# Optimization experiments

Hardware: AMD Instinct MI355X
Metric: run time of the kernel (lower is better)

The kernel has to match this reference:

```python
import jax, jax.numpy as jnp
import numpy as np

B, N, C = 32, 64, 128   # events, particles/event, channels (hidden==hidden2==out)
NUM_MAPS = 15           # bell_number(2+2)
E = B * N * N
LN_EPS = 1e-5


def setup_inputs() -> dict:
    key = jax.random.key(0)
    ks = jax.random.split(key, 8)
    x = jax.random.normal(ks[0], (E, C), jnp.float32)
    # complete graph with self-loops per event, nodes of event b are b*N..b*N+N-1
    node = np.arange(B * N, dtype=np.int32).reshape(B, N)
    src = np.repeat(node, N, axis=1).reshape(-1)            # i index per edge
    dst = np.tile(node, (1, N)).reshape(-1)                 # j index per edge
    edge_index = jnp.asarray(np.stack([src, dst]), jnp.int32)
    batch = jnp.asarray(np.repeat(np.arange(B, dtype=np.int32), N))
    # params: Linear(C->C), LayerNorm(C), factorized aggregator coeffs
    W_in = jax.random.normal(ks[1], (C, C), jnp.float32) / np.sqrt(C)
    b_in = jnp.zeros((C,), jnp.float32)
    ln_g = jnp.ones((C,), jnp.float32)
    ln_b = jnp.zeros((C,), jnp.float32)
    s0 = np.sqrt(3.0 / NUM_MAPS)
    s1 = np.sqrt(3.0 / C)
    c00 = jax.random.uniform(ks[2], (C, NUM_MAPS), jnp.float32, -s0, s0)
    c01 = jax.random.uniform(ks[3], (C, NUM_MAPS), jnp.float32, -s0, s0)
    c10 = jax.random.uniform(ks[4], (C, C), jnp.float32, -s1, s1)
    c11 = jax.random.uniform(ks[5], (C, C), jnp.float32, -s1, s1)
    return {"x": x, "edge_index": edge_index, "batch": batch,
            "W_in": W_in, "b_in": b_in, "ln_g": ln_g, "ln_b": ln_b,
            "c00": c00, "c01": c01, "c10": c10, "c11": c11}


def reference(x, edge_index, batch, W_in, b_in, ln_g, ln_b, c00, c01, c10, c11):
    # mlp: Linear -> GELU -> LayerNorm (this order, per ModuleList)
    h = x @ W_in.T + b_in
    h = jax.nn.gelu(h, approximate=False)
    mu = h.mean(-1, keepdims=True)
    var = ((h - mu) ** 2).mean(-1, keepdims=True)
    h = (h - mu) / jnp.sqrt(var + LN_EPS) * ln_g + ln_b

    # aggregate_2to2 with reduce='mean': 15 Eq(2->2) permutation-equivariant maps.
    # edge_index/batch describe complete graphs of N nodes per event -> dense view.
    t = h.reshape(B, N, N, C)                 # t[b,i,j,c]
    row = t.mean(axis=2)                      # [B,N,C] mean_j t[b,i,j]
    col = t.mean(axis=1)                      # [B,N,C] mean_i t[b,i,j]
    idx = jnp.arange(N)
    diag = t[:, idx, idx]                     # [B,N,C]
    trace = diag.mean(axis=1)                 # [B,C]
    tot = t.mean(axis=(1, 2))                 # [B,C]
    eye = jnp.eye(N, dtype=t.dtype)[None, :, :, None]

    # factorized coeffs [C_in?, C_out?, 15]; with C_in==C_out the flatten/linear in
    # the torch code makes the FIRST axis the output channel: out = sum map_m @ coeffs[:,:,m].T
    coeffs = c00[:, None, :] * c10[:, :, None] + c01[None, :, :] * c11[:, :, None]

    def proj(a, m):  # a[..., c] -> [..., o] with W[o, c] = coeffs[o, c, m]
        return jnp.einsum('...c,oc->...o', a, coeffs[:, :, m])

    out = proj(t, 0) + proj(t.swapaxes(1, 2), 1)
    out = out + proj(diag, 2)[:, :, None, :] + proj(diag, 3)[:, None, :, :]
    out = out + proj(row, 4)[:, :, None, :] + proj(row, 5)[:, None, :, :]
    out = out + proj(col, 6)[:, :, None, :] + proj(col, 7)[:, None, :, :]
    out = out + proj(trace, 8)[:, None, None, :] + proj(tot, 9)[:, None, None, :]
    out = out + eye * (proj(diag, 10)[:, :, None, :]
                       + proj(row, 11)[:, :, None, :]
                       + proj(col, 12)[:, :, None, :])
    out = out + eye * (proj(trace, 13)[:, None, None, :]
                       + proj(tot, 14)[:, None, None, :])

    return jax.nn.gelu(out.reshape(E, C), approximate=False)
```

## Files before the change

kernel.cpp:

```cpp
#include <hip/hip_runtime.h>
#include <hip/hip_bf16.h>


#define B_ 32
#define N_ 64
#define C_ 128
#define E_ (B_ * N_ * N_)
#define LN_EPS 1e-5f

typedef unsigned int u32;
typedef unsigned short u16;
typedef short bf16x8 __attribute__((ext_vector_type(8)));
typedef float f32x16 __attribute__((ext_vector_type(16)));

union FragU { uint4 u; bf16x8 v; };

__device__ inline float bf_u16(u16 u) { return __uint_as_float(((u32)u) << 16); }
__device__ inline u32 pack_bf2(float a, float b) {
    __hip_bfloat16 ha = __float2bfloat16(a), hb = __float2bfloat16(b);
    u16 ra = *reinterpret_cast<u16*>(&ha), rb = *reinterpret_cast<u16*>(&hb);
    return (u32)ra | ((u32)rb << 16);
}
__device__ inline u16 pack_bf1(float a) {
    __hip_bfloat16 ha = __float2bfloat16(a);
    return *reinterpret_cast<u16*>(&ha);
}
__device__ inline float b2f(__hip_bfloat16 v) { return __bfloat162float(v); }
__device__ inline float geluf(float v) {
    float v3 = v * v * v;
    float z = 0.7978845608f * fmaf(0.044715f, v3, v);
    float az = fabsf(z);
    float e = __expf(2.0f * az);
    float th = 1.0f - 2.0f / (e + 1.0f);
    th = copysignf(th, z);
    return 0.5f * v * (1.0f + th);
}
__device__ inline float ld1(const void* p, int i, int isbf) {
    if (isbf) return b2f(((const __hip_bfloat16*)p)[i]);
    return ((const float*)p)[i];
}
__device__ inline int bf_flag(const void* gp) {
    return (((const u32*)gp)[0] == 0x3F803F80u) ? 1 : 0;
}

#define O_T      ((size_t)0)
#define O_ROW    ((size_t)33554432)
#define O_DIAG   ((size_t)35651584)
#define O_CT     ((size_t)36732928)
#define O_WF     ((size_t)37715968)
#define O_CF     ((size_t)37748736)
#define O_U      ((size_t)37912576)
#define O_V      ((size_t)38961152)
#define O_DGN    ((size_t)40026112)
#define O_TT     ((size_t)41091328)

__global__ void pack_all(const void* __restrict__ W,
                         const void* __restrict__ c00, const void* __restrict__ c01,
                         const void* __restrict__ c10, const void* __restrict__ c11,
                         const void* __restrict__ gp,
                         uint4* __restrict__ WF, uint4* __restrict__ CF,
                         float* __restrict__ cT) {
    int isbf = bf_flag(gp);
    if (blockIdx.x < 24) {
        int idx = blockIdx.x * 256 + threadIdx.x;
        if (idx < 2048) {
            int l = idx & 63, s = (idx >> 6) & 7, ot = idx >> 9;
            int n = ot * 32 + (l & 31), k0 = s * 16 + (l >> 5) * 8;
            float v[8];
#pragma unroll
            for (int j = 0; j < 8; ++j) v[j] = ld1(W, n * 128 + k0 + j, isbf);
            uint4 o;
            o.x = pack_bf2(v[0], v[1]); o.y = pack_bf2(v[2], v[3]);
            o.z = pack_bf2(v[4], v[5]); o.w = pack_bf2(v[6], v[7]);
            WF[(s * 4 + ot) * 64 + l] = o;
        } else {
            int id2 = idx - 2048;
            int mat = id2 >> 11, r = id2 & 2047;
            int l = r & 63, s = (r >> 6) & 7, ot = r >> 9;
            int n = ot * 32 + (l & 31), k0 = s * 16 + (l >> 5) * 8;
            float v[8];
#pragma unroll
            for (int j = 0; j < 8; ++j) {
                int k = k0 + j;
                v[j] = ld1(c00, n * 15 + mat, isbf) * ld1(c10, n * 128 + k, isbf) +
                       ld1(c01, k * 15 + mat, isbf) * ld1(c11, n * 128 + k, isbf);
            }
            uint4 o;
            o.x = pack_bf2(v[0], v[1]); o.y = pack_bf2(v[2], v[3]);
            o.z = pack_bf2(v[4], v[5]); o.w = pack_bf2(v[6], v[7]);
            CF[mat * 2048 + (s * 4 + ot) * 64 + l] = o;
        }
    } else {
        int idx2 = (blockIdx.x - 24) * 256 + threadIdx.x;
        int m = idx2 >> 14, rem = idx2 & 16383;
        int c = rem >> 7, o = rem & 127;
        float val = ld1(c00, o * 15 + m, isbf) * ld1(c10, o * 128 + c, isbf) +
                    ld1(c01, c * 15 + m, isbf) * ld1(c11, o * 128 + c, isbf);
        cT[(m * 128 + c) * 128 + o] = val;
    }
}

__global__ void __launch_bounds__(256) gemm_ln_mfma(const void* __restrict__ x,
                                                    const uint4* __restrict__ WF,
                                                    const void* __restrict__ bp, const void* __restrict__ gp,
                                                    const void* __restrict__ lbp,
                                                    u16* __restrict__ t, u16* __restrict__ tT,
                                                    float* __restrict__ row_sum, float* __restrict__ diag) {
    __shared__ __align__(16) u16 tls[128 * 128];
    __shared__ float rsbuf[4][128];
    uint4* wfl = (uint4*)tls;
    int w = threadIdx.x >> 6, l = threadIdx.x & 63;
    int m = l & 31, hh = l >> 5;
    int isbf = bf_flag(gp);
    int e0 = blockIdx.x * 128;
    int arow = e0 + w * 32 + m;

#pragma unroll
    for (int k = 0; k < 8; ++k) {
        int idx = k * 256 + threadIdx.x;
        wfl[idx] = WF[idx];
    }

    FragU af[8];
    if (isbf) {
#pragma unroll
        for (int s = 0; s < 8; ++s)
            af[s].u = *(const uint4*)((const u16*)x + arow * 128 + s * 16 + hh * 8);
    } else {
        const float* xf = (const float*)x;
#pragma unroll
        for (int s = 0; s < 8; ++s) {
            int k0 = s * 16 + hh * 8;
            float4 f0 = *(const float4*)(xf + arow * 128 + k0);
            float4 f1 = *(const float4*)(xf + arow * 128 + k0 + 4);
            af[s].u.x = pack_bf2(f0.x, f0.y); af[s].u.y = pack_bf2(f0.z, f0.w);
            af[s].u.z = pack_bf2(f1.x, f1.y); af[s].u.w = pack_bf2(f1.z, f1.w);
        }
    }
    __syncthreads();

    f32x16 acc[4];
#pragma unroll
    for (int ot = 0; ot < 4; ++ot)
#pragma unroll
        for (int r = 0; r < 16; ++r) acc[ot][r] = 0.f;

#pragma unroll
    for (int s = 0; s < 8; ++s) {
#pragma unroll
        for (int ot = 0; ot < 4; ++ot) {
            FragU bf;
            bf.u = wfl[(s * 4 + ot) * 64 + l];
            acc[ot] = __builtin_amdgcn_mfma_f32_32x32x16_bf16(af[s].v, bf.v, acc[ot], 0, 0, 0);
        }
    }

    float bias[4], gsc[4], bof[4];
#pragma unroll
    for (int ot = 0; ot < 4; ++ot) {
        int o = ot * 32 + m;
        bias[ot] = ld1(bp, o, isbf);
        gsc[ot] = ld1(gp, o, isbf);
        bof[ot] = ld1(lbp, o, isbf);
    }
#pragma unroll
    for (int ot = 0; ot < 4; ++ot)
#pragma unroll
        for (int r = 0; r < 16; ++r) acc[ot][r] = geluf(acc[ot][r] + bias[ot]);

    __syncthreads();

    float rsum[4] = {0.f, 0.f, 0.f, 0.f};
#pragma unroll
    for (int r = 0; r < 16; ++r) {
        float s = acc[0][r] + acc[1][r] + acc[2][r] + acc[3][r];
        float s2 = acc[0][r] * acc[0][r] + acc[1][r] * acc[1][r] +
                   acc[2][r] * acc[2][r] + acc[3][r] * acc[3][r];
#pragma unroll
        for (int off = 1; off < 32; off <<= 1) {
            s += __shfl_xor(s, off);
            s2 += __shfl_xor(s2, off);
        }
        float mean = s * (1.0f / 128.0f);
        float var = s2 * (1.0f / 128.0f) - mean * mean;
        float rstd = rsqrtf(var + LN_EPS);
        int row = (r & 3) + 8 * (r >> 2) + 4 * hh;
#pragma unroll
        for (int ot = 0; ot < 4; ++ot) {
            int o = ot * 32 + m;
            float y = (acc[ot][r] - mean) * rstd * gsc[ot] + bof[ot];
            rsum[ot] += y;
            tls[(w * 32 + row) * 128 + o] = pack_bf1(y);
        }
    }
#pragma unroll
    for (int ot = 0; ot < 4; ++ot) {
        rsum[ot] += __shfl_xor(rsum[ot], 32);
        rsbuf[w][ot * 32 + m] = rsum[ot];
    }
    __syncthreads();

    int b = e0 >> 12, i0 = (e0 >> 6) & 63;
    {
        int p = threadIdx.x >> 7, c = threadIdx.x & 127;
        int ni = b * 64 + i0 + p;
        row_sum[ni * 128 + c] = rsbuf[2 * p][c] + rsbuf[2 * p + 1][c];
        diag[ni * 128 + c] = bf_u16(tls[(p * 64 + i0 + p) * 128 + c]);
    }
#pragma unroll
    for (int q = 0; q < 8; ++q) {
        int chunk = q * 256 + threadIdx.x;
        int row = chunk >> 4, c16 = chunk & 15;
        uint4 v = *(const uint4*)&tls[row * 128 + c16 * 8];
        *(uint4*)&t[(e0 + row) * 128 + c16 * 8] = v;
        int p = row >> 6, j = row & 63;
        int g = (b << 12) + (j << 6) + (i0 + p);
        *(uint4*)&tT[g * 128 + c16 * 8] = v;
    }
}

__global__ void __launch_bounds__(512) uvall_kernel(const u16* __restrict__ tT,
                                                    const float* __restrict__ row_sum,
                                                    const float* __restrict__ diag,
                                                    const float* __restrict__ cT,
                                                    float* __restrict__ U, float* __restrict__ V,
                                                    float* __restrict__ DgN) {
    __shared__ float dg[4][128], rm[4][128], cm[4][128];
    __shared__ float trs[128], tts[128];
    __shared__ float pU[4][4][128], pV[4][4][128], pD[4][4][128];
    __shared__ float paw[4][128], pad_[4][128];
    int b = blockIdx.x >> 4, n0 = (blockIdx.x & 15) * 4;
    int tid = threadIdx.x;
    int o = tid & 127, cq = tid >> 7;

    {
        int g = (b * 64 + n0 + cq) * 128 + o;
        dg[cq][o] = diag[g];
        rm[cq][o] = row_sum[g] * (1.0f / 64.0f);
    }
    float cs[4];
#pragma unroll
    for (int nn = 0; nn < 4; ++nn) {
        int base = ((b << 12) + ((n0 + nn) << 6) + cq * 16) * 128 + o;
        float s = 0.f;
#pragma unroll
        for (int i = 0; i < 16; ++i) s += bf_u16(tT[base + i * 128]);
        cs[nn] = s;
    }
    float tr = 0.f, tt = 0.f;
#pragma unroll
    for (int n = 0; n < 16; ++n) {
        int g = (b * 64 + cq * 16 + n) * 128 + o;
        tr += diag[g];
        tt += row_sum[g];
    }
#pragma unroll
    for (int nn = 0; nn < 4; ++nn) pU[cq][nn][o] = cs[nn];
    paw[cq][o] = tr;
    pad_[cq][o] = tt;
    __syncthreads();
    cm[cq][o] = (pU[0][cq][o] + pU[1][cq][o] + pU[2][cq][o] + pU[3][cq][o]) * (1.0f / 64.0f);
    if (cq == 0) trs[o] = (paw[0][o] + paw[1][o] + paw[2][o] + paw[3][o]) * (1.0f / 64.0f);
    if (cq == 1) tts[o] = (pad_[0][o] + pad_[1][o] + pad_[2][o] + pad_[3][o]) * (1.0f / 4096.0f);
    __syncthreads();

    float aU[4] = {0}, aV[4] = {0}, aD[4] = {0}, aw = 0.f, ad = 0.f;
    int c0 = cq * 32;
    for (int cc = 0; cc < 32; ++cc) {
        int c = c0 + cc;
        float c2 = cT[(2 * 128 + c) * 128 + o], c4 = cT[(4 * 128 + c) * 128 + o], c6 = cT[(6 * 128 + c) * 128 + o];
        float c3 = cT[(3 * 128 + c) * 128 + o], c5 = cT[(5 * 128 + c) * 128 + o], c7 = cT[(7 * 128 + c) * 128 + o];
        float cA = cT[(10 * 128 + c) * 128 + o], cB = cT[(11 * 128 + c) * 128 + o], cC = cT[(12 * 128 + c) * 128 + o];
        float c8 = cT[(8 * 128 + c) * 128 + o], c9 = cT[(9 * 128 + c) * 128 + o];
        float cD = cT[(13 * 128 + c) * 128 + o], cE = cT[(14 * 128 + c) * 128 + o];
        float trv = trs[c], ttv = tts[c];
        aw += c8 * trv + c9 * ttv;
        ad += cD * trv + cE * ttv;
#pragma unroll
        for (int nn = 0; nn < 4; ++nn) {
            float d = dg[nn][c], r = rm[nn][c], cl = cm[nn][c];
            aU[nn] += c2 * d + c4 * r + c6 * cl;
            aV[nn] += c3 * d + c5 * r + c7 * cl;
            aD[nn] += cA * d + cB * r + cC * cl;
        }
    }
#pragma unroll
    for (int nn = 0; nn < 4; ++nn) {
        pU[cq][nn][o] = aU[nn];
        pV[cq][nn][o] = aV[nn];
        pD[cq][nn][o] = aD[nn];
    }
    paw[cq][o] = aw;
    pad_[cq][o] = ad;
    __syncthreads();
    {
        int nn = cq;
        float u = pU[0][nn][o] + pU[1][nn][o] + pU[2][nn][o] + pU[3][nn][o];
        float v = pV[0][nn][o] + pV[1][nn][o] + pV[2][nn][o] + pV[3][nn][o];
        float d = pD[0][nn][o] + pD[1][nn][o] + pD[2][nn][o] + pD[3][nn][o];
        float w = paw[0][o] + paw[1][o] + paw[2][o] + paw[3][o];
        float a = pad_[0][o] + pad_[1][o] + pad_[2][o] + pad_[3][o];
        int g = (b * 64 + n0 + nn) * 128 + o;
        U[g] = u + w;
        V[g] = v;
        DgN[g] = d + a;
    }
}

__global__ void __launch_bounds__(256) final_mfma(const u16* __restrict__ t, const u16* __restrict__ tT,
                                                  const uint4* __restrict__ CF,
                                                  const float* __restrict__ U, const float* __restrict__ V,
                                                  const float* __restrict__ DgN, const void* __restrict__ gp,
                                                  void* __restrict__ outp) {
    __shared__ __align__(16) uint4 cfl[4096];
    u16* ols = (u16*)cfl;
    int w = threadIdx.x >> 6, l = threadIdx.x & 63;
    int m = l & 31, hh = l >> 5;
    int e0 = blockIdx.x * 128;
    int b = e0 >> 12;
    int i0 = (e0 >> 6) & 63;
    int iw = i0 + (w >> 1);
    int jA = (w & 1) * 32 + m;
    const u16* ai_base = t + (size_t)(e0 + w * 32 + m) * 128;
    const u16* aj_base = tT + (size_t)((b << 12) + (iw << 6) + jA) * 128;

#pragma unroll
    for (int k = 0; k < 16; ++k) {
        int idx = k * 256 + threadIdx.x;
        cfl[idx] = CF[idx];
    }

    FragU af[8], ag[8];
#pragma unroll
    for (int s = 0; s < 8; ++s) {
        int k0 = s * 16 + hh * 8;
        af[s].u = *(const uint4*)(ai_base + k0);
        ag[s].u = *(const uint4*)(aj_base + k0);
    }
    __syncthreads();

    f32x16 acc[4];
#pragma unroll
    for (int ot = 0; ot < 4; ++ot)
#pragma unroll
        for (int r = 0; r < 16; ++r) acc[ot][r] = 0.f;

#pragma unroll
    for (int s = 0; s < 8; ++s) {
#pragma unroll
        for (int ot = 0; ot < 4; ++ot) {
            FragU b0, b1;
            b0.u = cfl[(s * 4 + ot) * 64 + l];
            b1.u = cfl[2048 + (s * 4 + ot) * 64 + l];
            acc[ot] = __builtin_amdgcn_mfma_f32_32x32x16_bf16(af[s].v, b0.v, acc[ot], 0, 0, 0);
            acc[ot] = __builtin_amdgcn_mfma_f32_32x32x16_bf16(ag[s].v, b1.v, acc[ot], 0, 0, 0);
        }
    }

    int ni = b * 64 + iw;
    int isbf = bf_flag(gp);
    float uw[4], dg4[4];
#pragma unroll
    for (int ot = 0; ot < 4; ++ot) {
        int o = ot * 32 + m;
        uw[ot] = U[ni * 128 + o];
        dg4[ot] = DgN[ni * 128 + o];
    }
    if (isbf) {
        __syncthreads();
#pragma unroll
        for (int r = 0; r < 16; ++r) {
            int row = (r & 3) + 8 * (r >> 2) + 4 * hh;
            int jD = (w & 1) * 32 + row;
            int nj = b * 64 + jD;
            bool dia = (jD == iw);
#pragma unroll
            for (int ot = 0; ot < 4; ++ot) {
                int o = ot * 32 + m;
                float val = acc[ot][r] + uw[ot] + V[nj * 128 + o];
                if (dia) val += dg4[ot];
                ols[(w * 32 + row) * 128 + o] = pack_bf1(geluf(val));
            }
        }
        __syncthreads();
        u16* ob = (u16*)outp;
#pragma unroll
        for (int q = 0; q < 8; ++q) {
            int chunk = q * 256 + threadIdx.x;
            int row = chunk >> 4, c16 = chunk & 15;
            uint4 v = *(const uint4*)&ols[row * 128 + c16 * 8];
            *(uint4*)&ob[(e0 + row) * 128 + c16 * 8] = v;
        }
    } else {
        float* ob = (float*)outp;
#pragma unroll
        for (int r = 0; r < 16; ++r) {
            int row = (r & 3) + 8 * (r >> 2) + 4 * hh;
            int jD = (w & 1) * 32 + row;
            int e = e0 + w * 32 + row;
            int nj = b * 64 + jD;
            bool dia = (jD == iw);
#pragma unroll
            for (int ot = 0; ot < 4; ++ot) {
                int o = ot * 32 + m;
                float val = acc[ot][r] + uw[ot] + V[nj * 128 + o];
                if (dia) val += dg4[ot];
                ob[e * 128 + o] = geluf(val);
            }
        }
    }
}

extern "C" void kernel_launch(void* const* d_in, const int* in_sizes, int n_in,
                              void* d_out, int out_size, void* d_ws, size_t ws_size,
                              hipStream_t stream) {
    const void* x = d_in[0];
    const void* W = d_in[3];
    const void* bp = d_in[4];
    const void* gp = d_in[5];
    const void* lbp = d_in[6];
    const void* c00 = d_in[7];
    const void* c01 = d_in[8];
    const void* c10 = d_in[9];
    const void* c11 = d_in[10];

    char* ws = (char*)d_ws;
    u16* t16 = (u16*)(ws + O_T);
    u16* tT16 = (u16*)(ws + O_TT);
    float* row_sum = (float*)(ws + O_ROW);
    float* diag = (float*)(ws + O_DIAG);
    float* cT = (float*)(ws + O_CT);
    uint4* WF = (uint4*)(ws + O_WF);
    uint4* CF = (uint4*)(ws + O_CF);
    float* Uarr = (float*)(ws + O_U);
    float* Varr = (float*)(ws + O_V);
    float* DgN = (float*)(ws + O_DGN);

    pack_all<<<984, 256, 0, stream>>>(W, c00, c01, c10, c11, gp, WF, CF, cT);
    gemm_ln_mfma<<<E_ / 128, 256, 0, stream>>>(x, WF, bp, gp, lbp, t16, tT16, row_sum, diag);
    uvall_kernel<<<B_ * 16, 512, 0, stream>>>(tT16, row_sum, diag, cT, Uarr, Varr, DgN);
    final_mfma<<<E_ / 128, 256, 0, stream>>>(t16, tT16, CF, Uarr, Varr, DgN, gp, (void*)d_out);
}
```

Before: 211.6 us.

## Drop transposed activation copy, read strided t directly, halve final LDS footprint

Stops writing the transposed bf16 copy tT in the GEMM+LayerNorm kernel and makes the column-sum and final kernels gather transposed rows straight from t with strided addresses. This removes a full extra write and a read stream of the 16M-element intermediate. The final kernel now stages the two coefficient matrices one after the other in half-size shared memory, with extra barriers between them, which may raise occupancy. GELU is also rewritten to a cheaper exp2/rcp sigmoid-form tanh approximation. The trade-off is uncoalesced 256-byte-stride reads for the transposed operand and extra syncs.

```diff
diff --git a/kernel.cpp b/kernel.cpp
--- a/kernel.cpp
+++ b/kernel.cpp
@@ -27,13 +27,10 @@
 }
 __device__ inline float b2f(__hip_bfloat16 v) { return __bfloat162float(v); }
 __device__ inline float geluf(float v) {
-    float v3 = v * v * v;
-    float z = 0.7978845608f * fmaf(0.044715f, v3, v);
-    float az = fabsf(z);
-    float e = __expf(2.0f * az);
-    float th = 1.0f - 2.0f / (e + 1.0f);
-    th = copysignf(th, z);
-    return 0.5f * v * (1.0f + th);
+    float v2 = v * v;
+    float w = fmaf(0.044715f * v2, v, v);
+    float e = __builtin_amdgcn_exp2f(2.3022083f * w);
+    return v - v * __builtin_amdgcn_rcpf(e + 1.0f);
 }
 __device__ inline float ld1(const void* p, int i, int isbf) {
     if (isbf) return b2f(((const __hip_bfloat16*)p)[i]);
@@ -52,7 +49,6 @@
 #define O_U      ((size_t)37912576)
 #define O_V      ((size_t)38961152)
 #define O_DGN    ((size_t)40026112)
-#define O_TT     ((size_t)41091328)
 
 __global__ void pack_all(const void* __restrict__ W,
                          const void* __restrict__ c00, const void* __restrict__ c01,
@@ -104,7 +100,7 @@
                                                     const uint4* __restrict__ WF,
                                                     const void* __restrict__ bp, const void* __restrict__ gp,
                                                     const void* __restrict__ lbp,
-                                                    u16* __restrict__ t, u16* __restrict__ tT,
+                                                    u16* __restrict__ t,
                                                     float* __restrict__ row_sum, float* __restrict__ diag) {
     __shared__ __align__(16) u16 tls[128 * 128];
     __shared__ float rsbuf[4][128];
@@ -213,13 +209,10 @@
         int row = chunk >> 4, c16 = chunk & 15;
         uint4 v = *(const uint4*)&tls[row * 128 + c16 * 8];
         *(uint4*)&t[(e0 + row) * 128 + c16 * 8] = v;
-        int p = row >> 6, j = row & 63;
-        int g = (b << 12) + (j << 6) + (i0 + p);
-        *(uint4*)&tT[g * 128 + c16 * 8] = v;
-    }
-}
-
-__global__ void __launch_bounds__(512) uvall_kernel(const u16* __restrict__ tT,
+    }
+}
+
+__global__ void __launch_bounds__(512) uvall_kernel(const u16* __restrict__ t,
                                                     const float* __restrict__ row_sum,
                                                     const float* __restrict__ diag,
                                                     const float* __restrict__ cT,
@@ -241,10 +234,10 @@
     float cs[4];
 #pragma unroll
     for (int nn = 0; nn < 4; ++nn) {
-        int base = ((b << 12) + ((n0 + nn) << 6) + cq * 16) * 128 + o;
+        size_t base = (((size_t)(b << 12) + (n0 + nn)) << 7) + o + ((size_t)cq << 17);
         float s = 0.f;
 #pragma unroll
-        for (int i = 0; i < 16; ++i) s += bf_u16(tT[base + i * 128]);
+        for (int i = 0; i < 16; ++i) s += bf_u16(t[base + ((size_t)i << 13)]);
         cs[nn] = s;
     }
     float tr = 0.f, tt = 0.f;
@@ -307,12 +300,12 @@
     }
 }
 
-__global__ void __launch_bounds__(256) final_mfma(const u16* __restrict__ t, const u16* __restrict__ tT,
+__global__ void __launch_bounds__(256) final_mfma(const u16* __restrict__ t,
                                                   const uint4* __restrict__ CF,
                                                   const float* __restrict__ U, const float* __restrict__ V,
                                                   const float* __restrict__ DgN, const void* __restrict__ gp,
                                                   void* __restrict__ outp) {
-    __shared__ __align__(16) uint4 cfl[4096];
+    __shared__ __align__(16) uint4 cfl[2048];
     u16* ols = (u16*)cfl;
     int w = threadIdx.x >> 6, l = threadIdx.x & 63;
     int m = l & 31, hh = l >> 5;
@@ -322,10 +315,10 @@
     int iw = i0 + (w >> 1);
     int jA = (w & 1) * 32 + m;
     const u16* ai_base = t + (size_t)(e0 + w * 32 + m) * 128;
-    const u16* aj_base = tT + (size_t)((b << 12) + (iw << 6) + jA) * 128;
-
-#pragma unroll
-    for (int k = 0; k < 16; ++k) {
+    const u16* aj_base = t + (size_t)((b << 12) + (jA << 6) + iw) * 128;
+
+#pragma unroll
+    for (int k = 0; k < 8; ++k) {
         int idx = k * 256 + threadIdx.x;
         cfl[idx] = CF[idx];
     }
@@ -349,10 +342,24 @@
     for (int s = 0; s < 8; ++s) {
 #pragma unroll
         for (int ot = 0; ot < 4; ++ot) {
-            FragU b0, b1;
+            FragU b0;
             b0.u = cfl[(s * 4 + ot) * 64 + l];
-            b1.u = cfl[2048 + (s * 4 + ot) * 64 + l];
             acc[ot] = __builtin_amdgcn_mfma_f32_32x32x16_bf16(af[s].v, b0.v, acc[ot], 0, 0, 0);
+        }
+    }
+    __syncthreads();
+#pragma unroll
+    for (int k = 0; k < 8; ++k) {
+        int idx = k * 256 + threadIdx.x;
+        cfl[idx] = CF[2048 + idx];
+    }
+    __syncthreads();
+#pragma unroll
+    for (int s = 0; s < 8; ++s) {
+#pragma unroll
+        for (int ot = 0; ot < 4; ++ot) {
+            FragU b1;
+            b1.u = cfl[(s * 4 + ot) * 64 + l];
             acc[ot] = __builtin_amdgcn_mfma_f32_32x32x16_bf16(ag[s].v, b1.v, acc[ot], 0, 0, 0);
         }
     }
@@ -426,7 +433,6 @@
 
     char* ws = (char*)d_ws;
     u16* t16 = (u16*)(ws + O_T);
-    u16* tT16 = (u16*)(ws + O_TT);
     float* row_sum = (float*)(ws + O_ROW);
     float* diag = (float*)(ws + O_DIAG);
     float* cT = (float*)(ws + O_CT);
@@ -437,7 +443,7 @@
     float* DgN = (float*)(ws + O_DGN);
 
     pack_all<<<984, 256, 0, stream>>>(W, c00, c01, c10, c11, gp, WF, CF, cT);
-    gemm_ln_mfma<<<E_ / 128, 256, 0, stream>>>(x, WF, bp, gp, lbp, t16, tT16, row_sum, diag);
-    uvall_kernel<<<B_ * 16, 512, 0, stream>>>(tT16, row_sum, diag, cT, Uarr, Varr, DgN);
-    final_mfma<<<E_ / 128, 256, 0, stream>>>(t16, tT16, CF, Uarr, Varr, DgN, gp, (void*)d_out);
-}
+    gemm_ln_mfma<<<E_ / 128, 256, 0, stream>>>(x, WF, bp, gp, lbp, t16, row_sum, diag);
+    uvall_kernel<<<B_ * 16, 512, 0, stream>>>(t16, row_sum, diag, cT, Uarr, Varr, DgN);
+    final_mfma<<<E_ / 128, 256, 0, stream>>>(t16, CF, Uarr, Varr, DgN, gp, (void*)d_out);
+}
```

Result: faster. 199.8 us (-5.6%).
